# Kernel optimization log

Measured on AMD Instinct MI355X. Metric: run time of the kernel, lower is better.

Reference implementation:

```python
import jax, jax.numpy as jnp
import numpy as np

V = 100000  # num graph nodes
E = 800000  # num edges (avg degree 8)
B = 16      # batch
C = 16      # in == hidden == out channels (forced by residual adds)
K = 4       # Chebyshev order
EPS = 1e-5


def setup_inputs() -> dict:
    key = jax.random.key(0)
    ks = jax.random.split(key, 8)
    x = jax.random.normal(ks[0], (B, C, V), jnp.float32)
    edge_src = jax.random.randint(ks[1], (E,), 0, V, dtype=jnp.int32)
    edge_dst = jax.random.randint(ks[2], (E,), 0, V, dtype=jnp.int32)
    # small positive weights keep the Chebyshev recursion numerically tame
    edge_w = jax.random.uniform(ks[3], (E,), jnp.float32) * 0.1
    weights = jax.random.normal(ks[4], (6, K, C, C), jnp.float32) * (1.0 / np.sqrt(K * C))
    biases = jax.random.normal(ks[5], (6, C), jnp.float32) * 0.01
    gamma = jnp.ones((5, C), jnp.float32)
    beta = jnp.zeros((5, C), jnp.float32)
    return {"x": x, "edge_w": edge_w, "weights": weights, "biases": biases,
            "gamma": gamma, "beta": beta, "edge_src": edge_src, "edge_dst": edge_dst}


def reference(x, edge_w, weights, biases, gamma, beta, edge_src, edge_dst):
    def lap(xf):  # normalized laplacian apply: (2/lmax)*L - I with lmax=2 -> L - I; xf: (V, F)
        msg = xf[edge_src] * edge_w[:, None]
        return jax.ops.segment_sum(msg, edge_dst, num_segments=V) - xf

    def cheb(xin, w, b):  # xin: (B, Cin, V), w: (K, Cin, Cout), b: (Cout,)
        Cin = xin.shape[1]
        xf = xin.transpose(2, 0, 1).reshape(V, B * Cin)  # (V, B*Cin)
        x0 = xf
        xs = [x0]
        x1 = lap(x0)
        xs.append(x1)
        for _ in range(K - 2):
            x2 = 2.0 * lap(x1) - x0
            xs.append(x2)
            x0, x1 = x1, x2
        xk = jnp.stack(xs).reshape(K, V, B, Cin)
        out = jnp.einsum('kvbi,kio->bov', xk, w) + b[None, :, None]
        return out  # (B, Cout, V)

    def bn(xin, g, bt):  # BatchNorm1d over (B, C, V): stats over (B, V)
        mean = xin.mean(axis=(0, 2), keepdims=True)
        var = xin.var(axis=(0, 2), keepdims=True)
        return (xin - mean) * jax.lax.rsqrt(var + EPS) * g[None, :, None] + bt[None, :, None]

    def resblock(xin, i, bni):
        h = jax.nn.relu(cheb(xin, weights[2 * i], biases[2 * i]))
        h = bn(h, gamma[bni], beta[bni])
        h = cheb(h, weights[2 * i + 1], biases[2 * i + 1])
        return jax.nn.relu(h + xin)

    out = resblock(x, 0, 0)
    out = bn(out, gamma[3], beta[3])
    out = resblock(out, 1, 1)
    out = bn(out, gamma[4], beta[4])
    out = resblock(out, 2, 2)
    pooled = out.max(axis=2)  # MaxPool1d(num_nodes) + squeeze -> (B, C)
    return jax.nn.softmax(pooled, axis=1)
```

## Files before the change

kernel.cpp:

```cpp
#include <hip/hip_runtime.h>
#include <hip/hip_fp16.h>
#include <cstdint>

#define CAP 32
#define WAVES 4

typedef __half half_t;

__device__ __forceinline__ float4 ldh4(const half_t* p) {
  uint2 u = *reinterpret_cast<const uint2*>(p);
  __half2 h0 = *reinterpret_cast<const __half2*>(&u.x);
  __half2 h1 = *reinterpret_cast<const __half2*>(&u.y);
  float2 f0 = __half22float2(h0);
  float2 f1 = __half22float2(h1);
  return make_float4(f0.x, f0.y, f1.x, f1.y);
}

__device__ __forceinline__ void sth4(half_t* p, float x, float y, float z, float w) {
  __half2 h0 = __floats2half2_rn(x, y);
  __half2 h1 = __floats2half2_rn(z, w);
  uint2 u;
  u.x = *reinterpret_cast<unsigned int*>(&h0);
  u.y = *reinterpret_cast<unsigned int*>(&h1);
  *reinterpret_cast<uint2*>(p) = u;
}

__global__ __launch_bounds__(256) void transpose_kernel(
    const float* __restrict__ in, half_t* __restrict__ out, int V) {
  __shared__ float t[32][33];
  const int f0 = blockIdx.y * 32;
  const int v0 = blockIdx.x * 32;
  const int tid = threadIdx.x;
  const int fi = tid >> 5;
  const int vi = tid & 31;
#pragma unroll
  for (int k = 0; k < 4; ++k) {
    int f = fi + 8 * k;
    t[f][vi] = in[(size_t)(f0 + f) * V + (v0 + vi)];
  }
  __syncthreads();
  const int vl = tid >> 5;
  const int fl = tid & 31;
#pragma unroll
  for (int k = 0; k < 4; ++k) {
    int v = vl + 8 * k;
    out[(size_t)(v0 + v) * 256 + (f0 + fl)] = __float2half_rn(t[fl][v]);
  }
}

__global__ __launch_bounds__(256) void init_slots(int2* __restrict__ slots, int total) {
  int i = blockIdx.x * 256 + threadIdx.x;
  if (i < total) slots[i] = make_int2(i >> 5, 0);
}

__global__ __launch_bounds__(256) void fill_kernel(
    const int* __restrict__ src, const int* __restrict__ dst,
    const float* __restrict__ w, int* __restrict__ cursor,
    int2* __restrict__ slots, int E) {
  int e = blockIdx.x * 256 + threadIdx.x;
  if (e >= E) return;
  int d = dst[e];
  int pos = atomicAdd(&cursor[d], 1);
  if (pos < CAP) slots[(size_t)d * CAP + pos] = make_int2(src[e], __float_as_int(w[e]));
}

template <int PASS, int EPI>
__global__ __launch_bounds__(256) void cheb_pass(
    const half_t* __restrict__ G, const half_t* __restrict__ Pv,
    half_t* __restrict__ D, half_t* __restrict__ O,
    const half_t* __restrict__ resid,
    const int2* __restrict__ slots, const int* __restrict__ cnt,
    const float* __restrict__ Wl, const float* __restrict__ bl,
    float* __restrict__ statsBuf, int V) {
  __shared__ float xl[WAVES][272];
  __shared__ float wl[512];
  const int tid = threadIdx.x;
  if (PASS == 1) {
    wl[tid] = Wl[tid];
    wl[256 + tid] = Wl[256 + tid];
  } else if (PASS == 2) {
    wl[tid] = Wl[512 + tid];
  } else {
    wl[tid] = Wl[768 + tid];
  }
  __syncthreads();
  const int wave = tid >> 6, lane = tid & 63;
  const int v = blockIdx.x * WAVES + wave;
  if (v >= V) return;
  const int f0 = lane << 2;
  const size_t rowoff = (((size_t)v) << 8) + f0;

  int2 myslot = slots[((size_t)v << 5) + (lane & 31)];
  float4 g = ldh4(G + rowoff);
  float4 p = make_float4(0.f, 0.f, 0.f, 0.f);
  if (PASS != 1) p = ldh4(Pv + rowoff);

  int n = cnt[v];
  n = n > CAP ? CAP : n;
  int n8 = (n + 7) & ~7;

  float4 acc = make_float4(0.f, 0.f, 0.f, 0.f);
  for (int base = 0; base < n8; base += 8) {
    const half_t* ap[8];
    float w[8];
#pragma unroll
    for (int j = 0; j < 8; ++j) {
      int s = __shfl(myslot.x, base + j);
      w[j] = __int_as_float(__shfl(myslot.y, base + j));
      ap[j] = G + (((size_t)s) << 8) + f0;
    }
    float4 a[8];
#pragma unroll
    for (int j = 0; j < 8; ++j) a[j] = ldh4(ap[j]);
#pragma unroll
    for (int j = 0; j < 8; ++j) {
      acc.x = fmaf(w[j], a[j].x, acc.x);
      acc.y = fmaf(w[j], a[j].y, acc.y);
      acc.z = fmaf(w[j], a[j].z, acc.z);
      acc.w = fmaf(w[j], a[j].w, acc.w);
    }
  }

  float4 xn;
  if (PASS == 1) {
    xn.x = acc.x - g.x; xn.y = acc.y - g.y; xn.z = acc.z - g.z; xn.w = acc.w - g.w;
  } else {
    xn.x = 2.f * (acc.x - g.x) - p.x;
    xn.y = 2.f * (acc.y - g.y) - p.y;
    xn.z = 2.f * (acc.z - g.z) - p.z;
    xn.w = 2.f * (acc.w - g.w) - p.w;
  }
  if (PASS != 3) {
    sth4(D + rowoff, xn.x, xn.y, xn.z, xn.w);
  }
  const int b = lane >> 2;
  const int oc = (lane & 3) << 2;
  float* xw = xl[wave];
  const int sbase = f0 + b;
  float o[4];
  if (PASS == 1) {
    o[0] = bl[oc + 0]; o[1] = bl[oc + 1]; o[2] = bl[oc + 2]; o[3] = bl[oc + 3];
    xw[sbase + 0] = g.x; xw[sbase + 1] = g.y; xw[sbase + 2] = g.z; xw[sbase + 3] = g.w;
    __builtin_amdgcn_wave_barrier();
    const float* xb = xw + b * 17;
#pragma unroll
    for (int i = 0; i < 16; ++i) {
      float xi = xb[i];
      o[0] = fmaf(xi, wl[i * 16 + oc + 0], o[0]);
      o[1] = fmaf(xi, wl[i * 16 + oc + 1], o[1]);
      o[2] = fmaf(xi, wl[i * 16 + oc + 2], o[2]);
      o[3] = fmaf(xi, wl[i * 16 + oc + 3], o[3]);
    }
    __builtin_amdgcn_wave_barrier();
  } else {
    o[0] = o[1] = o[2] = o[3] = 0.f;
  }
  xw[sbase + 0] = xn.x; xw[sbase + 1] = xn.y; xw[sbase + 2] = xn.z; xw[sbase + 3] = xn.w;
  __builtin_amdgcn_wave_barrier();
  {
    const float* xb = xw + b * 17;
    const float* wm = (PASS == 1) ? (wl + 256) : wl;
#pragma unroll
    for (int i = 0; i < 16; ++i) {
      float xi = xb[i];
      o[0] = fmaf(xi, wm[i * 16 + oc + 0], o[0]);
      o[1] = fmaf(xi, wm[i * 16 + oc + 1], o[1]);
      o[2] = fmaf(xi, wm[i * 16 + oc + 2], o[2]);
      o[3] = fmaf(xi, wm[i * 16 + oc + 3], o[3]);
    }
  }
  half_t* op = O + rowoff;
  if (PASS == 1) {
    sth4(op, o[0], o[1], o[2], o[3]);
  } else if (PASS == 2) {
    float4 c4 = ldh4(op);
    sth4(op, o[0] + c4.x, o[1] + c4.y, o[2] + c4.z, o[3] + c4.w);
  } else {
    float4 c4 = ldh4(op);
    o[0] += c4.x; o[1] += c4.y; o[2] += c4.z; o[3] += c4.w;
    if (EPI >= 2) {
      float4 r = ldh4(resid + rowoff);
      o[0] += r.x; o[1] += r.y; o[2] += r.z; o[3] += r.w;
    }
    o[0] = fmaxf(o[0], 0.f); o[1] = fmaxf(o[1], 0.f);
    o[2] = fmaxf(o[2], 0.f); o[3] = fmaxf(o[3], 0.f);
    sth4(op, o[0], o[1], o[2], o[3]);
    if (EPI == 1 || EPI == 2) {
      float s0 = o[0], s1 = o[1], s2 = o[2], s3 = o[3];
      float q0 = o[0] * o[0], q1 = o[1] * o[1], q2 = o[2] * o[2], q3 = o[3] * o[3];
#pragma unroll
      for (int d = 4; d < 64; d <<= 1) {
        s0 += __shfl_xor(s0, d); s1 += __shfl_xor(s1, d);
        s2 += __shfl_xor(s2, d); s3 += __shfl_xor(s3, d);
        q0 += __shfl_xor(q0, d); q1 += __shfl_xor(q1, d);
        q2 += __shfl_xor(q2, d); q3 += __shfl_xor(q3, d);
      }
      if (lane < 4) {
        float* sb = statsBuf + ((blockIdx.x & 63) << 5);
        atomicAdd(&sb[(lane << 2) + 0], s0);
        atomicAdd(&sb[(lane << 2) + 1], s1);
        atomicAdd(&sb[(lane << 2) + 2], s2);
        atomicAdd(&sb[(lane << 2) + 3], s3);
        atomicAdd(&sb[16 + (lane << 2) + 0], q0);
        atomicAdd(&sb[16 + (lane << 2) + 1], q1);
        atomicAdd(&sb[16 + (lane << 2) + 2], q2);
        atomicAdd(&sb[16 + (lane << 2) + 3], q3);
      }
    }
  }
}

__global__ void bn_finalize(const float* __restrict__ sb,
                            const float* __restrict__ gamma,
                            const float* __restrict__ beta,
                            float* __restrict__ affine, float invN) {
  int c = threadIdx.x;
  if (c >= 16) return;
  float s = 0.f, q = 0.f;
  for (int k = 0; k < 64; ++k) { s += sb[k * 32 + c]; q += sb[k * 32 + 16 + c]; }
  float mean = s * invN;
  float var = q * invN - mean * mean;
  float inv = rsqrtf(var + 1e-5f);
  float A = gamma[c] * inv;
  float B = beta[c] - mean * A;
  affine[c] = A;
  affine[16 + c] = B;
}

__global__ __launch_bounds__(256) void bn_apply(half_t* __restrict__ X,
                                                const float* __restrict__ affine,
                                                size_t NT) {
  size_t i0 = ((size_t)blockIdx.x * 256 + threadIdx.x) * 8;
  size_t stride = (size_t)gridDim.x * 256 * 8;
  float a[8], bb[8];
#pragma unroll
  for (int j = 0; j < 8; ++j) {
    int c = (int)((i0 + j) & 15);
    a[j] = affine[c];
    bb[j] = affine[16 + c];
  }
  for (size_t i = i0; i < NT; i += stride) {
    uint4 u = *reinterpret_cast<uint4*>(X + i);
    __half2* h = reinterpret_cast<__half2*>(&u);
#pragma unroll
    for (int j = 0; j < 4; ++j) {
      float2 f = __half22float2(h[j]);
      f.x = fmaf(a[2 * j], f.x, bb[2 * j]);
      f.y = fmaf(a[2 * j + 1], f.y, bb[2 * j + 1]);
      h[j] = __floats2half2_rn(f.x, f.y);
    }
    *reinterpret_cast<uint4*>(X + i) = u;
  }
}

__global__ __launch_bounds__(256) void pool_kernel(const half_t* __restrict__ X,
                                                   float* __restrict__ part, int V) {
  int t = threadIdx.x;
  float m = -3.402823466e38f;
  for (int v = blockIdx.x; v < V; v += gridDim.x) {
    m = fmaxf(m, __half2float(X[(((size_t)v) << 8) + t]));
  }
  part[blockIdx.x * 256 + t] = m;
}

__global__ __launch_bounds__(256) void pool_finish(const float* __restrict__ part,
                                                   float* __restrict__ out) {
  int t = threadIdx.x;
  float m = -3.402823466e38f;
  for (int k = 0; k < 256; ++k) m = fmaxf(m, part[k * 256 + t]);
  __shared__ float pm[256];
  __shared__ float mx[16], sm[16];
  pm[t] = m;
  __syncthreads();
  if (t < 16) {
    float M = -3.402823466e38f;
    for (int c = 0; c < 16; ++c) M = fmaxf(M, pm[t * 16 + c]);
    float S = 0.f;
    for (int c = 0; c < 16; ++c) S += expf(pm[t * 16 + c] - M);
    mx[t] = M;
    sm[t] = S;
  }
  __syncthreads();
  out[t] = expf(pm[t] - mx[t >> 4]) / sm[t >> 4];
}

__global__ void sentinel_kernel(float* out, float val) {
  out[threadIdx.x] = val;
}

extern "C" void kernel_launch(void* const* d_in, const int* in_sizes, int n_in,
                              void* d_out, int out_size, void* d_ws, size_t ws_size,
                              hipStream_t stream) {
  const float* x       = (const float*)d_in[0];
  const float* edge_w  = (const float*)d_in[1];
  const float* weights = (const float*)d_in[2];
  const float* biases  = (const float*)d_in[3];
  const float* gamma   = (const float*)d_in[4];
  const float* beta    = (const float*)d_in[5];
  const int*   esrc    = (const int*)d_in[6];
  const int*   edst    = (const int*)d_in[7];

  const int V = in_sizes[0] / 256;
  const int E = in_sizes[1];
  const size_t NT = (size_t)V * 256;

  char* wsp = (char*)d_ws;
  auto carve = [&](size_t bytes) {
    char* p = wsp;
    wsp += (bytes + 255) & ~(size_t)255;
    return p;
  };
  half_t* P[4];
  for (int i = 0; i < 4; ++i) P[i] = (half_t*)carve(NT * sizeof(half_t));
  int2*  slots  = (int2*)carve((size_t)V * CAP * sizeof(int2));
  int*   cursor = (int*)carve((size_t)V * sizeof(int));
  float* stats  = (float*)carve(5 * 64 * 32 * sizeof(float));
  float* affine = (float*)carve(5 * 32 * sizeof(float));
  float* part   = (float*)carve(256 * 256 * sizeof(float));
  size_t needed = (size_t)(wsp - (char*)d_ws);
  if (needed > ws_size) {
    sentinel_kernel<<<1, 256, 0, stream>>>((float*)d_out, 100.0f + (float)(needed >> 20));
    return;
  }

  hipMemsetAsync(cursor, 0, (size_t)V * sizeof(int), stream);
  hipMemsetAsync(stats, 0, 5 * 64 * 32 * sizeof(float), stream);

  const int totalSlots = V * CAP;
  init_slots<<<(totalSlots + 255) / 256, 256, 0, stream>>>(slots, totalSlots);

  dim3 tg(V / 32, 8, 1);
  transpose_kernel<<<tg, 256, 0, stream>>>(x, P[0], V);
  fill_kernel<<<(E + 255) / 256, 256, 0, stream>>>(esrc, edst, edge_w, cursor, slots, E);

  const int nb = (V + WAVES - 1) / WAVES;
  const float invN = 1.f / (16.f * (float)V);

  half_t *C = P[0], *X = P[1], *Y = P[2], *Z = P[3];
  for (int blk = 0; blk < 3; ++blk) {
    const float* WA = weights + (size_t)(2 * blk) * 1024;
    const float* WB = weights + (size_t)(2 * blk + 1) * 1024;
    const float* bA = biases + (2 * blk) * 16;
    const float* bB = biases + (2 * blk + 1) * 16;
    float* stA = stats + blk * 2048;
    float* afA = affine + blk * 32;
    cheb_pass<1, 0><<<nb, 256, 0, stream>>>(C, nullptr, X, Y, nullptr, slots, cursor, WA, bA, nullptr, V);
    cheb_pass<2, 0><<<nb, 256, 0, stream>>>(X, C, Z, Y, nullptr, slots, cursor, WA, nullptr, nullptr, V);
    cheb_pass<3, 1><<<nb, 256, 0, stream>>>(Z, X, nullptr, Y, nullptr, slots, cursor, WA, nullptr, stA, V);
    bn_finalize<<<1, 16, 0, stream>>>(stA, gamma + blk * 16, beta + blk * 16, afA, invN);
    bn_apply<<<2048, 256, 0, stream>>>(Y, afA, NT);
    cheb_pass<1, 0><<<nb, 256, 0, stream>>>(Y, nullptr, X, Z, nullptr, slots, cursor, WB, bB, nullptr, V);
    cheb_pass<2, 0><<<nb, 256, 0, stream>>>(X, Y, Y, Z, nullptr, slots, cursor, WB, nullptr, nullptr, V);
    if (blk < 2) {
      float* stI = stats + (3 + blk) * 2048;
      float* afI = affine + (3 + blk) * 32;
      cheb_pass<3, 2><<<nb, 256, 0, stream>>>(Y, X, nullptr, Z, C, slots, cursor, WB, nullptr, stI, V);
      bn_finalize<<<1, 16, 0, stream>>>(stI, gamma + (3 + blk) * 16, beta + (3 + blk) * 16, afI, invN);
      bn_apply<<<2048, 256, 0, stream>>>(Z, afI, NT);
    } else {
      cheb_pass<3, 3><<<nb, 256, 0, stream>>>(Y, X, nullptr, Z, C, slots, cursor, WB, nullptr, nullptr, V);
    }
    half_t* oC = C; half_t* oY = Y; half_t* oZ = Z;
    C = oZ; Y = oC; Z = oY;
  }
  pool_kernel<<<256, 256, 0, stream>>>(C, part, V);
  pool_finish<<<1, 256, 0, stream>>>(part, (float*)d_out);
}
```

Measured before the change: 2.279 ms.

## Fold BatchNorm affine into Chebyshev passes and process two nodes per wave

The separate bn_apply kernels are removed. The BN scale and shift is folded algebraically into the first two Chebyshev passes through the row sum of edge weights, and into the residual read, so the un-normalized buffer is consumed directly. Each wave now handles two vertices, which gives more independent gathers in flight and halves the block count. The output-accumulator load is also hoisted before the gather. This saves two full read-write sweeps over the feature tensor per block. In exchange it adds per-pass arithmetic, raises register pressure, and lets the two vertices in a wave diverge when their degrees differ.

```diff
diff --git a/kernel.cpp b/kernel.cpp
--- a/kernel.cpp
+++ b/kernel.cpp
@@ -64,6 +64,11 @@
   if (pos < CAP) slots[(size_t)d * CAP + pos] = make_int2(src[e], __float_as_int(w[e]));
 }
 
+__global__ void ident_affine(float* aff) {
+  int c = threadIdx.x;
+  if (c < 16) { aff[c] = 1.f; aff[16 + c] = 0.f; }
+}
+
 template <int PASS, int EPI>
 __global__ __launch_bounds__(256) void cheb_pass(
     const half_t* __restrict__ G, const half_t* __restrict__ Pv,
@@ -71,8 +76,8 @@
     const half_t* __restrict__ resid,
     const int2* __restrict__ slots, const int* __restrict__ cnt,
     const float* __restrict__ Wl, const float* __restrict__ bl,
-    float* __restrict__ statsBuf, int V) {
-  __shared__ float xl[WAVES][272];
+    const float* __restrict__ aff, float* __restrict__ statsBuf, int V) {
+  __shared__ float xl[WAVES][2][272];
   __shared__ float wl[512];
   const int tid = threadIdx.x;
   if (PASS == 1) {
@@ -85,126 +90,211 @@
   }
   __syncthreads();
   const int wave = tid >> 6, lane = tid & 63;
-  const int v = blockIdx.x * WAVES + wave;
-  if (v >= V) return;
+  const int va = blockIdx.x * (WAVES * 2) + wave * 2;
+  if (va >= V) return;
+  const int vb = va + 1;
   const int f0 = lane << 2;
-  const size_t rowoff = (((size_t)v) << 8) + f0;
-
-  int2 myslot = slots[((size_t)v << 5) + (lane & 31)];
-  float4 g = ldh4(G + rowoff);
-  float4 p = make_float4(0.f, 0.f, 0.f, 0.f);
-  if (PASS != 1) p = ldh4(Pv + rowoff);
-
-  int n = cnt[v];
-  n = n > CAP ? CAP : n;
-  int n8 = (n + 7) & ~7;
-
-  float4 acc = make_float4(0.f, 0.f, 0.f, 0.f);
-  for (int base = 0; base < n8; base += 8) {
-    const half_t* ap[8];
-    float w[8];
-#pragma unroll
-    for (int j = 0; j < 8; ++j) {
-      int s = __shfl(myslot.x, base + j);
-      w[j] = __int_as_float(__shfl(myslot.y, base + j));
-      ap[j] = G + (((size_t)s) << 8) + f0;
-    }
-    float4 a[8];
-#pragma unroll
-    for (int j = 0; j < 8; ++j) a[j] = ldh4(ap[j]);
-#pragma unroll
-    for (int j = 0; j < 8; ++j) {
-      acc.x = fmaf(w[j], a[j].x, acc.x);
-      acc.y = fmaf(w[j], a[j].y, acc.y);
-      acc.z = fmaf(w[j], a[j].z, acc.z);
-      acc.w = fmaf(w[j], a[j].w, acc.w);
-    }
-  }
-
-  float4 xn;
+  const int c0 = f0 & 15;
+  const size_t rowa = (((size_t)va) << 8) + f0;
+  const size_t rowb = (((size_t)vb) << 8) + f0;
+
+  float4 A4 = *reinterpret_cast<const float4*>(aff + c0);
+  float4 B4 = *reinterpret_cast<const float4*>(aff + 16 + c0);
+
+  size_t sidx = (lane < 32) ? ((((size_t)va) << 5) + lane)
+                            : ((((size_t)vb) << 5) + (lane - 32));
+  int2 slv = slots[sidx];
+  float4 ga = ldh4(G + rowa);
+  float4 gb = ldh4(G + rowb);
+  float4 pa = make_float4(0.f, 0.f, 0.f, 0.f), pb = pa;
+  float4 oa = pa, ob = pa;
+  if (PASS != 1) {
+    pa = ldh4(Pv + rowa);
+    pb = ldh4(Pv + rowb);
+    oa = ldh4(O + rowa);
+    ob = ldh4(O + rowb);
+  }
+  int na = cnt[va]; na = na > CAP ? CAP : na;
+  int nb = cnt[vb]; nb = nb > CAP ? CAP : nb;
+  int na8 = (na + 7) & ~7;
+  int nb8 = (nb + 7) & ~7;
+  int nmax = na8 > nb8 ? na8 : nb8;
+
+  float4 acca = make_float4(0.f, 0.f, 0.f, 0.f);
+  float4 accb = acca;
+  float swa = 0.f, swb = 0.f;
+  for (int base = 0; base < nmax; base += 8) {
+    bool da = base < na8, db = base < nb8;
+    float wa[8], wb[8];
+    const half_t* apa[8];
+    const half_t* apb[8];
+    if (da) {
+#pragma unroll
+      for (int j = 0; j < 8; ++j) {
+        int s = __shfl(slv.x, base + j);
+        wa[j] = __int_as_float(__shfl(slv.y, base + j));
+        apa[j] = G + (((size_t)s) << 8) + f0;
+      }
+    }
+    if (db) {
+#pragma unroll
+      for (int j = 0; j < 8; ++j) {
+        int s = __shfl(slv.x, 32 + base + j);
+        wb[j] = __int_as_float(__shfl(slv.y, 32 + base + j));
+        apb[j] = G + (((size_t)s) << 8) + f0;
+      }
+    }
+    float4 aa[8], ab[8];
+    if (da) {
+#pragma unroll
+      for (int j = 0; j < 8; ++j) aa[j] = ldh4(apa[j]);
+    }
+    if (db) {
+#pragma unroll
+      for (int j = 0; j < 8; ++j) ab[j] = ldh4(apb[j]);
+    }
+    if (da) {
+#pragma unroll
+      for (int j = 0; j < 8; ++j) {
+        acca.x = fmaf(wa[j], aa[j].x, acca.x);
+        acca.y = fmaf(wa[j], aa[j].y, acca.y);
+        acca.z = fmaf(wa[j], aa[j].z, acca.z);
+        acca.w = fmaf(wa[j], aa[j].w, acca.w);
+        if (PASS == 1) swa += wa[j];
+      }
+    }
+    if (db) {
+#pragma unroll
+      for (int j = 0; j < 8; ++j) {
+        accb.x = fmaf(wb[j], ab[j].x, accb.x);
+        accb.y = fmaf(wb[j], ab[j].y, accb.y);
+        accb.z = fmaf(wb[j], ab[j].z, accb.z);
+        accb.w = fmaf(wb[j], ab[j].w, accb.w);
+        if (PASS == 1) swb += wb[j];
+      }
+    }
+  }
+
+  float4 xna, xnb, gya, gyb;
   if (PASS == 1) {
-    xn.x = acc.x - g.x; xn.y = acc.y - g.y; xn.z = acc.z - g.z; xn.w = acc.w - g.w;
+    gya.x = fmaf(A4.x, ga.x, B4.x); gya.y = fmaf(A4.y, ga.y, B4.y);
+    gya.z = fmaf(A4.z, ga.z, B4.z); gya.w = fmaf(A4.w, ga.w, B4.w);
+    gyb.x = fmaf(A4.x, gb.x, B4.x); gyb.y = fmaf(A4.y, gb.y, B4.y);
+    gyb.z = fmaf(A4.z, gb.z, B4.z); gyb.w = fmaf(A4.w, gb.w, B4.w);
+    xna.x = A4.x * (acca.x - ga.x) + B4.x * (swa - 1.f);
+    xna.y = A4.y * (acca.y - ga.y) + B4.y * (swa - 1.f);
+    xna.z = A4.z * (acca.z - ga.z) + B4.z * (swa - 1.f);
+    xna.w = A4.w * (acca.w - ga.w) + B4.w * (swa - 1.f);
+    xnb.x = A4.x * (accb.x - gb.x) + B4.x * (swb - 1.f);
+    xnb.y = A4.y * (accb.y - gb.y) + B4.y * (swb - 1.f);
+    xnb.z = A4.z * (accb.z - gb.z) + B4.z * (swb - 1.f);
+    xnb.w = A4.w * (accb.w - gb.w) + B4.w * (swb - 1.f);
+  } else if (PASS == 2) {
+    xna.x = 2.f * (acca.x - ga.x) - fmaf(A4.x, pa.x, B4.x);
+    xna.y = 2.f * (acca.y - ga.y) - fmaf(A4.y, pa.y, B4.y);
+    xna.z = 2.f * (acca.z - ga.z) - fmaf(A4.z, pa.z, B4.z);
+    xna.w = 2.f * (acca.w - ga.w) - fmaf(A4.w, pa.w, B4.w);
+    xnb.x = 2.f * (accb.x - gb.x) - fmaf(A4.x, pb.x, B4.x);
+    xnb.y = 2.f * (accb.y - gb.y) - fmaf(A4.y, pb.y, B4.y);
+    xnb.z = 2.f * (accb.z - gb.z) - fmaf(A4.z, pb.z, B4.z);
+    xnb.w = 2.f * (accb.w - gb.w) - fmaf(A4.w, pb.w, B4.w);
   } else {
-    xn.x = 2.f * (acc.x - g.x) - p.x;
-    xn.y = 2.f * (acc.y - g.y) - p.y;
-    xn.z = 2.f * (acc.z - g.z) - p.z;
-    xn.w = 2.f * (acc.w - g.w) - p.w;
+    xna.x = 2.f * (acca.x - ga.x) - pa.x;
+    xna.y = 2.f * (acca.y - ga.y) - pa.y;
+    xna.z = 2.f * (acca.z - ga.z) - pa.z;
+    xna.w = 2.f * (acca.w - ga.w) - pa.w;
+    xnb.x = 2.f * (accb.x - gb.x) - pb.x;
+    xnb.y = 2.f * (accb.y - gb.y) - pb.y;
+    xnb.z = 2.f * (accb.z - gb.z) - pb.z;
+    xnb.w = 2.f * (accb.w - gb.w) - pb.w;
   }
   if (PASS != 3) {
-    sth4(D + rowoff, xn.x, xn.y, xn.z, xn.w);
-  }
+    sth4(D + rowa, xna.x, xna.y, xna.z, xna.w);
+    sth4(D + rowb, xnb.x, xnb.y, xnb.z, xnb.w);
+  }
+
   const int b = lane >> 2;
   const int oc = (lane & 3) << 2;
-  float* xw = xl[wave];
   const int sbase = f0 + b;
-  float o[4];
-  if (PASS == 1) {
-    o[0] = bl[oc + 0]; o[1] = bl[oc + 1]; o[2] = bl[oc + 2]; o[3] = bl[oc + 3];
-    xw[sbase + 0] = g.x; xw[sbase + 1] = g.y; xw[sbase + 2] = g.z; xw[sbase + 3] = g.w;
+#pragma unroll
+  for (int t = 0; t < 2; ++t) {
+    float4 xn = t ? xnb : xna;
+    float4 gy = t ? gyb : gya;
+    float4 oprev = t ? ob : oa;
+    size_t row = t ? rowb : rowa;
+    float* xw = xl[wave][t];
+    float o[4];
+    if (PASS == 1) {
+      o[0] = bl[oc + 0]; o[1] = bl[oc + 1]; o[2] = bl[oc + 2]; o[3] = bl[oc + 3];
+      xw[sbase + 0] = gy.x; xw[sbase + 1] = gy.y;
+      xw[sbase + 2] = gy.z; xw[sbase + 3] = gy.w;
+      __builtin_amdgcn_wave_barrier();
+      const float* xb = xw + b * 17;
+#pragma unroll
+      for (int i = 0; i < 16; ++i) {
+        float xi = xb[i];
+        o[0] = fmaf(xi, wl[i * 16 + oc + 0], o[0]);
+        o[1] = fmaf(xi, wl[i * 16 + oc + 1], o[1]);
+        o[2] = fmaf(xi, wl[i * 16 + oc + 2], o[2]);
+        o[3] = fmaf(xi, wl[i * 16 + oc + 3], o[3]);
+      }
+      __builtin_amdgcn_wave_barrier();
+    } else {
+      o[0] = o[1] = o[2] = o[3] = 0.f;
+    }
+    xw[sbase + 0] = xn.x; xw[sbase + 1] = xn.y;
+    xw[sbase + 2] = xn.z; xw[sbase + 3] = xn.w;
     __builtin_amdgcn_wave_barrier();
-    const float* xb = xw + b * 17;
-#pragma unroll
-    for (int i = 0; i < 16; ++i) {
-      float xi = xb[i];
-      o[0] = fmaf(xi, wl[i * 16 + oc + 0], o[0]);
-      o[1] = fmaf(xi, wl[i * 16 + oc + 1], o[1]);
-      o[2] = fmaf(xi, wl[i * 16 + oc + 2], o[2]);
-      o[3] = fmaf(xi, wl[i * 16 + oc + 3], o[3]);
-    }
-    __builtin_amdgcn_wave_barrier();
-  } else {
-    o[0] = o[1] = o[2] = o[3] = 0.f;
-  }
-  xw[sbase + 0] = xn.x; xw[sbase + 1] = xn.y; xw[sbase + 2] = xn.z; xw[sbase + 3] = xn.w;
-  __builtin_amdgcn_wave_barrier();
-  {
-    const float* xb = xw + b * 17;
-    const float* wm = (PASS == 1) ? (wl + 256) : wl;
-#pragma unroll
-    for (int i = 0; i < 16; ++i) {
-      float xi = xb[i];
-      o[0] = fmaf(xi, wm[i * 16 + oc + 0], o[0]);
-      o[1] = fmaf(xi, wm[i * 16 + oc + 1], o[1]);
-      o[2] = fmaf(xi, wm[i * 16 + oc + 2], o[2]);
-      o[3] = fmaf(xi, wm[i * 16 + oc + 3], o[3]);
-    }
-  }
-  half_t* op = O + rowoff;
-  if (PASS == 1) {
-    sth4(op, o[0], o[1], o[2], o[3]);
-  } else if (PASS == 2) {
-    float4 c4 = ldh4(op);
-    sth4(op, o[0] + c4.x, o[1] + c4.y, o[2] + c4.z, o[3] + c4.w);
-  } else {
-    float4 c4 = ldh4(op);
-    o[0] += c4.x; o[1] += c4.y; o[2] += c4.z; o[3] += c4.w;
-    if (EPI >= 2) {
-      float4 r = ldh4(resid + rowoff);
-      o[0] += r.x; o[1] += r.y; o[2] += r.z; o[3] += r.w;
-    }
-    o[0] = fmaxf(o[0], 0.f); o[1] = fmaxf(o[1], 0.f);
-    o[2] = fmaxf(o[2], 0.f); o[3] = fmaxf(o[3], 0.f);
-    sth4(op, o[0], o[1], o[2], o[3]);
-    if (EPI == 1 || EPI == 2) {
-      float s0 = o[0], s1 = o[1], s2 = o[2], s3 = o[3];
-      float q0 = o[0] * o[0], q1 = o[1] * o[1], q2 = o[2] * o[2], q3 = o[3] * o[3];
-#pragma unroll
-      for (int d = 4; d < 64; d <<= 1) {
-        s0 += __shfl_xor(s0, d); s1 += __shfl_xor(s1, d);
-        s2 += __shfl_xor(s2, d); s3 += __shfl_xor(s3, d);
-        q0 += __shfl_xor(q0, d); q1 += __shfl_xor(q1, d);
-        q2 += __shfl_xor(q2, d); q3 += __shfl_xor(q3, d);
-      }
-      if (lane < 4) {
-        float* sb = statsBuf + ((blockIdx.x & 63) << 5);
-        atomicAdd(&sb[(lane << 2) + 0], s0);
-        atomicAdd(&sb[(lane << 2) + 1], s1);
-        atomicAdd(&sb[(lane << 2) + 2], s2);
-        atomicAdd(&sb[(lane << 2) + 3], s3);
-        atomicAdd(&sb[16 + (lane << 2) + 0], q0);
-        atomicAdd(&sb[16 + (lane << 2) + 1], q1);
-        atomicAdd(&sb[16 + (lane << 2) + 2], q2);
-        atomicAdd(&sb[16 + (lane << 2) + 3], q3);
+    {
+      const float* xb = xw + b * 17;
+      const float* wm = (PASS == 1) ? (wl + 256) : wl;
+#pragma unroll
+      for (int i = 0; i < 16; ++i) {
+        float xi = xb[i];
+        o[0] = fmaf(xi, wm[i * 16 + oc + 0], o[0]);
+        o[1] = fmaf(xi, wm[i * 16 + oc + 1], o[1]);
+        o[2] = fmaf(xi, wm[i * 16 + oc + 2], o[2]);
+        o[3] = fmaf(xi, wm[i * 16 + oc + 3], o[3]);
+      }
+    }
+    half_t* op = O + row;
+    if (PASS == 1) {
+      sth4(op, o[0], o[1], o[2], o[3]);
+    } else if (PASS == 2) {
+      sth4(op, o[0] + oprev.x, o[1] + oprev.y, o[2] + oprev.z, o[3] + oprev.w);
+    } else {
+      o[0] += oprev.x; o[1] += oprev.y; o[2] += oprev.z; o[3] += oprev.w;
+      if (EPI >= 2) {
+        float4 r = ldh4(resid + row);
+        o[0] = fmaf(A4.x, r.x, B4.x) + o[0];
+        o[1] = fmaf(A4.y, r.y, B4.y) + o[1];
+        o[2] = fmaf(A4.z, r.z, B4.z) + o[2];
+        o[3] = fmaf(A4.w, r.w, B4.w) + o[3];
+      }
+      o[0] = fmaxf(o[0], 0.f); o[1] = fmaxf(o[1], 0.f);
+      o[2] = fmaxf(o[2], 0.f); o[3] = fmaxf(o[3], 0.f);
+      sth4(op, o[0], o[1], o[2], o[3]);
+      if (EPI == 1 || EPI == 2) {
+        float s0 = o[0], s1 = o[1], s2 = o[2], s3 = o[3];
+        float q0 = o[0] * o[0], q1 = o[1] * o[1], q2 = o[2] * o[2], q3 = o[3] * o[3];
+#pragma unroll
+        for (int d = 4; d < 64; d <<= 1) {
+          s0 += __shfl_xor(s0, d); s1 += __shfl_xor(s1, d);
+          s2 += __shfl_xor(s2, d); s3 += __shfl_xor(s3, d);
+          q0 += __shfl_xor(q0, d); q1 += __shfl_xor(q1, d);
+          q2 += __shfl_xor(q2, d); q3 += __shfl_xor(q3, d);
+        }
+        if (lane < 4) {
+          float* sb = statsBuf + ((blockIdx.x & 63) << 5);
+          atomicAdd(&sb[(lane << 2) + 0], s0);
+          atomicAdd(&sb[(lane << 2) + 1], s1);
+          atomicAdd(&sb[(lane << 2) + 2], s2);
+          atomicAdd(&sb[(lane << 2) + 3], s3);
+          atomicAdd(&sb[16 + (lane << 2) + 0], q0);
+          atomicAdd(&sb[16 + (lane << 2) + 1], q1);
+          atomicAdd(&sb[16 + (lane << 2) + 2], q2);
+          atomicAdd(&sb[16 + (lane << 2) + 3], q3);
+        }
       }
     }
   }
@@ -225,32 +315,6 @@
   float B = beta[c] - mean * A;
   affine[c] = A;
   affine[16 + c] = B;
-}
-
-__global__ __launch_bounds__(256) void bn_apply(half_t* __restrict__ X,
-                                                const float* __restrict__ affine,
-                                                size_t NT) {
-  size_t i0 = ((size_t)blockIdx.x * 256 + threadIdx.x) * 8;
-  size_t stride = (size_t)gridDim.x * 256 * 8;
-  float a[8], bb[8];
-#pragma unroll
-  for (int j = 0; j < 8; ++j) {
-    int c = (int)((i0 + j) & 15);
-    a[j] = affine[c];
-    bb[j] = affine[16 + c];
-  }
-  for (size_t i = i0; i < NT; i += stride) {
-    uint4 u = *reinterpret_cast<uint4*>(X + i);
-    __half2* h = reinterpret_cast<__half2*>(&u);
-#pragma unroll
-    for (int j = 0; j < 4; ++j) {
-      float2 f = __half22float2(h[j]);
-      f.x = fmaf(a[2 * j], f.x, bb[2 * j]);
-      f.y = fmaf(a[2 * j + 1], f.y, bb[2 * j + 1]);
-      h[j] = __floats2half2_rn(f.x, f.y);
-    }
-    *reinterpret_cast<uint4*>(X + i) = u;
-  }
 }
 
 __global__ __launch_bounds__(256) void pool_kernel(const half_t* __restrict__ X,
@@ -315,25 +379,27 @@
   int2*  slots  = (int2*)carve((size_t)V * CAP * sizeof(int2));
   int*   cursor = (int*)carve((size_t)V * sizeof(int));
   float* stats  = (float*)carve(5 * 64 * 32 * sizeof(float));
-  float* affine = (float*)carve(5 * 32 * sizeof(float));
+  float* affine = (float*)carve(6 * 32 * sizeof(float));
   float* part   = (float*)carve(256 * 256 * sizeof(float));
   size_t needed = (size_t)(wsp - (char*)d_ws);
   if (needed > ws_size) {
     sentinel_kernel<<<1, 256, 0, stream>>>((float*)d_out, 100.0f + (float)(needed >> 20));
     return;
   }
+  float* ident = affine + 5 * 32;
 
   hipMemsetAsync(cursor, 0, (size_t)V * sizeof(int), stream);
   hipMemsetAsync(stats, 0, 5 * 64 * 32 * sizeof(float), stream);
 
   const int totalSlots = V * CAP;
   init_slots<<<(totalSlots + 255) / 256, 256, 0, stream>>>(slots, totalSlots);
+  ident_affine<<<1, 16, 0, stream>>>(ident);
 
   dim3 tg(V / 32, 8, 1);
   transpose_kernel<<<tg, 256, 0, stream>>>(x, P[0], V);
   fill_kernel<<<(E + 255) / 256, 256, 0, stream>>>(esrc, edst, edge_w, cursor, slots, E);
 
-  const int nb = (V + WAVES - 1) / WAVES;
+  const int nb = (V + WAVES * 2 - 1) / (WAVES * 2);
   const float invN = 1.f / (16.f * (float)V);
 
   half_t *C = P[0], *X = P[1], *Y = P[2], *Z = P[3];
@@ -342,23 +408,22 @@
     const float* WB = weights + (size_t)(2 * blk + 1) * 1024;
     const float* bA = biases + (2 * blk) * 16;
     const float* bB = biases + (2 * blk + 1) * 16;
-    float* stA = stats + blk * 2048;
-    float* afA = affine + blk * 32;
-    cheb_pass<1, 0><<<nb, 256, 0, stream>>>(C, nullptr, X, Y, nullptr, slots, cursor, WA, bA, nullptr, V);
-    cheb_pass<2, 0><<<nb, 256, 0, stream>>>(X, C, Z, Y, nullptr, slots, cursor, WA, nullptr, nullptr, V);
-    cheb_pass<3, 1><<<nb, 256, 0, stream>>>(Z, X, nullptr, Y, nullptr, slots, cursor, WA, nullptr, stA, V);
-    bn_finalize<<<1, 16, 0, stream>>>(stA, gamma + blk * 16, beta + blk * 16, afA, invN);
-    bn_apply<<<2048, 256, 0, stream>>>(Y, afA, NT);
-    cheb_pass<1, 0><<<nb, 256, 0, stream>>>(Y, nullptr, X, Z, nullptr, slots, cursor, WB, bB, nullptr, V);
-    cheb_pass<2, 0><<<nb, 256, 0, stream>>>(X, Y, Y, Z, nullptr, slots, cursor, WB, nullptr, nullptr, V);
+    float* stA  = stats + blk * 2048;
+    float* afMid = affine + blk * 32;
+    const float* afIn = (blk == 0) ? ident : (affine + (2 + blk) * 32);
+    cheb_pass<1, 0><<<nb, 256, 0, stream>>>(C, nullptr, X, Y, nullptr, slots, cursor, WA, bA, afIn, nullptr, V);
+    cheb_pass<2, 0><<<nb, 256, 0, stream>>>(X, C, Z, Y, nullptr, slots, cursor, WA, nullptr, afIn, nullptr, V);
+    cheb_pass<3, 1><<<nb, 256, 0, stream>>>(Z, X, nullptr, Y, nullptr, slots, cursor, WA, nullptr, ident, stA, V);
+    bn_finalize<<<1, 16, 0, stream>>>(stA, gamma + blk * 16, beta + blk * 16, afMid, invN);
+    cheb_pass<1, 0><<<nb, 256, 0, stream>>>(Y, nullptr, X, Z, nullptr, slots, cursor, WB, bB, afMid, nullptr, V);
+    cheb_pass<2, 0><<<nb, 256, 0, stream>>>(X, Y, Y, Z, nullptr, slots, cursor, WB, nullptr, afMid, nullptr, V);
     if (blk < 2) {
       float* stI = stats + (3 + blk) * 2048;
       float* afI = affine + (3 + blk) * 32;
-      cheb_pass<3, 2><<<nb, 256, 0, stream>>>(Y, X, nullptr, Z, C, slots, cursor, WB, nullptr, stI, V);
+      cheb_pass<3, 2><<<nb, 256, 0, stream>>>(Y, X, nullptr, Z, C, slots, cursor, WB, nullptr, afIn, stI, V);
       bn_finalize<<<1, 16, 0, stream>>>(stI, gamma + (3 + blk) * 16, beta + (3 + blk) * 16, afI, invN);
-      bn_apply<<<2048, 256, 0, stream>>>(Z, afI, NT);
     } else {
-      cheb_pass<3, 3><<<nb, 256, 0, stream>>>(Y, X, nullptr, Z, C, slots, cursor, WB, nullptr, nullptr, V);
+      cheb_pass<3, 3><<<nb, 256, 0, stream>>>(Y, X, nullptr, Z, C, slots, cursor, WB, nullptr, afIn, nullptr, V);
     }
     half_t* oC = C; half_t* oY = Y; half_t* oZ = Z;
     C = oZ; Y = oC; Z = oY;
```

After: 2.527 ms. +10.9%, slower.

## Fold batchnorm affine into Chebyshev passes and drop standalone bn_apply kernels

Applied to the files above, without the earlier changes.

Removes the separate bn_apply kernels. The BN affine (A*x+B) is applied lazily inside the next block's Chebyshev passes instead. Because the Laplacian is linear, pass 1 folds the affine into the gathered neighbour sum using the per-node sum of edge weights, pass 2 applies it to the previous term, and the residual path applies it when the residual is read. It also prefetches the output accumulator early and raises the launch-bounds occupancy hint. This saves a full read and write of the activation tensor per BN, at the cost of a few extra FMAs and some added register pressure.

```diff
diff --git a/kernel.cpp b/kernel.cpp
--- a/kernel.cpp
+++ b/kernel.cpp
@@ -64,14 +64,19 @@
   if (pos < CAP) slots[(size_t)d * CAP + pos] = make_int2(src[e], __float_as_int(w[e]));
 }
 
+__global__ void ident_affine(float* aff) {
+  int c = threadIdx.x;
+  if (c < 16) { aff[c] = 1.f; aff[16 + c] = 0.f; }
+}
+
 template <int PASS, int EPI>
-__global__ __launch_bounds__(256) void cheb_pass(
+__global__ __launch_bounds__(256, 8) void cheb_pass(
     const half_t* __restrict__ G, const half_t* __restrict__ Pv,
     half_t* __restrict__ D, half_t* __restrict__ O,
     const half_t* __restrict__ resid,
     const int2* __restrict__ slots, const int* __restrict__ cnt,
     const float* __restrict__ Wl, const float* __restrict__ bl,
-    float* __restrict__ statsBuf, int V) {
+    const float* __restrict__ aff, float* __restrict__ statsBuf, int V) {
   __shared__ float xl[WAVES][272];
   __shared__ float wl[512];
   const int tid = threadIdx.x;
@@ -88,18 +93,27 @@
   const int v = blockIdx.x * WAVES + wave;
   if (v >= V) return;
   const int f0 = lane << 2;
+  const int c0 = f0 & 15;
   const size_t rowoff = (((size_t)v) << 8) + f0;
+
+  float4 A4 = *reinterpret_cast<const float4*>(aff + c0);
+  float4 B4 = *reinterpret_cast<const float4*>(aff + 16 + c0);
 
   int2 myslot = slots[((size_t)v << 5) + (lane & 31)];
   float4 g = ldh4(G + rowoff);
   float4 p = make_float4(0.f, 0.f, 0.f, 0.f);
-  if (PASS != 1) p = ldh4(Pv + rowoff);
+  float4 oprev = p;
+  if (PASS != 1) {
+    p = ldh4(Pv + rowoff);
+    oprev = ldh4(O + rowoff);
+  }
 
   int n = cnt[v];
   n = n > CAP ? CAP : n;
   int n8 = (n + 7) & ~7;
 
   float4 acc = make_float4(0.f, 0.f, 0.f, 0.f);
+  float sw = 0.f;
   for (int base = 0; base < n8; base += 8) {
     const half_t* ap[8];
     float w[8];
@@ -118,12 +132,24 @@
       acc.y = fmaf(w[j], a[j].y, acc.y);
       acc.z = fmaf(w[j], a[j].z, acc.z);
       acc.w = fmaf(w[j], a[j].w, acc.w);
-    }
-  }
-
-  float4 xn;
+      if (PASS == 1) sw += w[j];
+    }
+  }
+
+  float4 xn, gy;
   if (PASS == 1) {
-    xn.x = acc.x - g.x; xn.y = acc.y - g.y; xn.z = acc.z - g.z; xn.w = acc.w - g.w;
+    gy.x = fmaf(A4.x, g.x, B4.x); gy.y = fmaf(A4.y, g.y, B4.y);
+    gy.z = fmaf(A4.z, g.z, B4.z); gy.w = fmaf(A4.w, g.w, B4.w);
+    float swm1 = sw - 1.f;
+    xn.x = A4.x * (acc.x - g.x) + B4.x * swm1;
+    xn.y = A4.y * (acc.y - g.y) + B4.y * swm1;
+    xn.z = A4.z * (acc.z - g.z) + B4.z * swm1;
+    xn.w = A4.w * (acc.w - g.w) + B4.w * swm1;
+  } else if (PASS == 2) {
+    xn.x = 2.f * (acc.x - g.x) - fmaf(A4.x, p.x, B4.x);
+    xn.y = 2.f * (acc.y - g.y) - fmaf(A4.y, p.y, B4.y);
+    xn.z = 2.f * (acc.z - g.z) - fmaf(A4.z, p.z, B4.z);
+    xn.w = 2.f * (acc.w - g.w) - fmaf(A4.w, p.w, B4.w);
   } else {
     xn.x = 2.f * (acc.x - g.x) - p.x;
     xn.y = 2.f * (acc.y - g.y) - p.y;
@@ -133,6 +159,7 @@
   if (PASS != 3) {
     sth4(D + rowoff, xn.x, xn.y, xn.z, xn.w);
   }
+
   const int b = lane >> 2;
   const int oc = (lane & 3) << 2;
   float* xw = xl[wave];
@@ -140,7 +167,8 @@
   float o[4];
   if (PASS == 1) {
     o[0] = bl[oc + 0]; o[1] = bl[oc + 1]; o[2] = bl[oc + 2]; o[3] = bl[oc + 3];
-    xw[sbase + 0] = g.x; xw[sbase + 1] = g.y; xw[sbase + 2] = g.z; xw[sbase + 3] = g.w;
+    xw[sbase + 0] = gy.x; xw[sbase + 1] = gy.y;
+    xw[sbase + 2] = gy.z; xw[sbase + 3] = gy.w;
     __builtin_amdgcn_wave_barrier();
     const float* xb = xw + b * 17;
 #pragma unroll
@@ -155,7 +183,8 @@
   } else {
     o[0] = o[1] = o[2] = o[3] = 0.f;
   }
-  xw[sbase + 0] = xn.x; xw[sbase + 1] = xn.y; xw[sbase + 2] = xn.z; xw[sbase + 3] = xn.w;
+  xw[sbase + 0] = xn.x; xw[sbase + 1] = xn.y;
+  xw[sbase + 2] = xn.z; xw[sbase + 3] = xn.w;
   __builtin_amdgcn_wave_barrier();
   {
     const float* xb = xw + b * 17;
@@ -173,14 +202,15 @@
   if (PASS == 1) {
     sth4(op, o[0], o[1], o[2], o[3]);
   } else if (PASS == 2) {
-    float4 c4 = ldh4(op);
-    sth4(op, o[0] + c4.x, o[1] + c4.y, o[2] + c4.z, o[3] + c4.w);
+    sth4(op, o[0] + oprev.x, o[1] + oprev.y, o[2] + oprev.z, o[3] + oprev.w);
   } else {
-    float4 c4 = ldh4(op);
-    o[0] += c4.x; o[1] += c4.y; o[2] += c4.z; o[3] += c4.w;
+    o[0] += oprev.x; o[1] += oprev.y; o[2] += oprev.z; o[3] += oprev.w;
     if (EPI >= 2) {
       float4 r = ldh4(resid + rowoff);
-      o[0] += r.x; o[1] += r.y; o[2] += r.z; o[3] += r.w;
+      o[0] += fmaf(A4.x, r.x, B4.x);
+      o[1] += fmaf(A4.y, r.y, B4.y);
+      o[2] += fmaf(A4.z, r.z, B4.z);
+      o[3] += fmaf(A4.w, r.w, B4.w);
     }
     o[0] = fmaxf(o[0], 0.f); o[1] = fmaxf(o[1], 0.f);
     o[2] = fmaxf(o[2], 0.f); o[3] = fmaxf(o[3], 0.f);
@@ -227,32 +257,6 @@
   affine[16 + c] = B;
 }
 
-__global__ __launch_bounds__(256) void bn_apply(half_t* __restrict__ X,
-                                                const float* __restrict__ affine,
-                                                size_t NT) {
-  size_t i0 = ((size_t)blockIdx.x * 256 + threadIdx.x) * 8;
-  size_t stride = (size_t)gridDim.x * 256 * 8;
-  float a[8], bb[8];
-#pragma unroll
-  for (int j = 0; j < 8; ++j) {
-    int c = (int)((i0 + j) & 15);
-    a[j] = affine[c];
-    bb[j] = affine[16 + c];
-  }
-  for (size_t i = i0; i < NT; i += stride) {
-    uint4 u = *reinterpret_cast<uint4*>(X + i);
-    __half2* h = reinterpret_cast<__half2*>(&u);
-#pragma unroll
-    for (int j = 0; j < 4; ++j) {
-      float2 f = __half22float2(h[j]);
-      f.x = fmaf(a[2 * j], f.x, bb[2 * j]);
-      f.y = fmaf(a[2 * j + 1], f.y, bb[2 * j + 1]);
-      h[j] = __floats2half2_rn(f.x, f.y);
-    }
-    *reinterpret_cast<uint4*>(X + i) = u;
-  }
-}
-
 __global__ __launch_bounds__(256) void pool_kernel(const half_t* __restrict__ X,
                                                    float* __restrict__ part, int V) {
   int t = threadIdx.x;
@@ -315,19 +319,21 @@
   int2*  slots  = (int2*)carve((size_t)V * CAP * sizeof(int2));
   int*   cursor = (int*)carve((size_t)V * sizeof(int));
   float* stats  = (float*)carve(5 * 64 * 32 * sizeof(float));
-  float* affine = (float*)carve(5 * 32 * sizeof(float));
+  float* affine = (float*)carve(6 * 32 * sizeof(float));
   float* part   = (float*)carve(256 * 256 * sizeof(float));
   size_t needed = (size_t)(wsp - (char*)d_ws);
   if (needed > ws_size) {
     sentinel_kernel<<<1, 256, 0, stream>>>((float*)d_out, 100.0f + (float)(needed >> 20));
     return;
   }
+  float* ident = affine + 5 * 32;
 
   hipMemsetAsync(cursor, 0, (size_t)V * sizeof(int), stream);
   hipMemsetAsync(stats, 0, 5 * 64 * 32 * sizeof(float), stream);
 
   const int totalSlots = V * CAP;
   init_slots<<<(totalSlots + 255) / 256, 256, 0, stream>>>(slots, totalSlots);
+  ident_affine<<<1, 16, 0, stream>>>(ident);
 
   dim3 tg(V / 32, 8, 1);
   transpose_kernel<<<tg, 256, 0, stream>>>(x, P[0], V);
@@ -342,23 +348,22 @@
     const float* WB = weights + (size_t)(2 * blk + 1) * 1024;
     const float* bA = biases + (2 * blk) * 16;
     const float* bB = biases + (2 * blk + 1) * 16;
-    float* stA = stats + blk * 2048;
-    float* afA = affine + blk * 32;
-    cheb_pass<1, 0><<<nb, 256, 0, stream>>>(C, nullptr, X, Y, nullptr, slots, cursor, WA, bA, nullptr, V);
-    cheb_pass<2, 0><<<nb, 256, 0, stream>>>(X, C, Z, Y, nullptr, slots, cursor, WA, nullptr, nullptr, V);
-    cheb_pass<3, 1><<<nb, 256, 0, stream>>>(Z, X, nullptr, Y, nullptr, slots, cursor, WA, nullptr, stA, V);
-    bn_finalize<<<1, 16, 0, stream>>>(stA, gamma + blk * 16, beta + blk * 16, afA, invN);
-    bn_apply<<<2048, 256, 0, stream>>>(Y, afA, NT);
-    cheb_pass<1, 0><<<nb, 256, 0, stream>>>(Y, nullptr, X, Z, nullptr, slots, cursor, WB, bB, nullptr, V);
-    cheb_pass<2, 0><<<nb, 256, 0, stream>>>(X, Y, Y, Z, nullptr, slots, cursor, WB, nullptr, nullptr, V);
+    float* stA  = stats + blk * 2048;
+    float* afMid = affine + blk * 32;
+    const float* afIn = (blk == 0) ? ident : (affine + (2 + blk) * 32);
+    cheb_pass<1, 0><<<nb, 256, 0, stream>>>(C, nullptr, X, Y, nullptr, slots, cursor, WA, bA, afIn, nullptr, V);
+    cheb_pass<2, 0><<<nb, 256, 0, stream>>>(X, C, Z, Y, nullptr, slots, cursor, WA, nullptr, afIn, nullptr, V);
+    cheb_pass<3, 1><<<nb, 256, 0, stream>>>(Z, X, nullptr, Y, nullptr, slots, cursor, WA, nullptr, ident, stA, V);
+    bn_finalize<<<1, 16, 0, stream>>>(stA, gamma + blk * 16, beta + blk * 16, afMid, invN);
+    cheb_pass<1, 0><<<nb, 256, 0, stream>>>(Y, nullptr, X, Z, nullptr, slots, cursor, WB, bB, afMid, nullptr, V);
+    cheb_pass<2, 0><<<nb, 256, 0, stream>>>(X, Y, Y, Z, nullptr, slots, cursor, WB, nullptr, afMid, nullptr, V);
     if (blk < 2) {
       float* stI = stats + (3 + blk) * 2048;
       float* afI = affine + (3 + blk) * 32;
-      cheb_pass<3, 2><<<nb, 256, 0, stream>>>(Y, X, nullptr, Z, C, slots, cursor, WB, nullptr, stI, V);
+      cheb_pass<3, 2><<<nb, 256, 0, stream>>>(Y, X, nullptr, Z, C, slots, cursor, WB, nullptr, afIn, stI, V);
       bn_finalize<<<1, 16, 0, stream>>>(stI, gamma + (3 + blk) * 16, beta + (3 + blk) * 16, afI, invN);
-      bn_apply<<<2048, 256, 0, stream>>>(Z, afI, NT);
     } else {
-      cheb_pass<3, 3><<<nb, 256, 0, stream>>>(Y, X, nullptr, Z, C, slots, cursor, WB, nullptr, nullptr, V);
+      cheb_pass<3, 3><<<nb, 256, 0, stream>>>(Y, X, nullptr, Z, C, slots, cursor, WB, nullptr, afIn, nullptr, V);
     }
     half_t* oC = C; half_t* oY = Y; half_t* oZ = Z;
     C = oZ; Y = oC; Z = oY;
```

New measurement: 2.537 ms. 1.11x slower.
